# Performance work log

Measured on AMD Instinct MI355X. Metric: run time of the kernel, lower is better.

The kernel has to match this reference:

```python
import jax, jax.numpy as jnp
import numpy as np

B, H, S, D = 2048, 1024, 32768, 64  # batch, hidden_dim, memory_slots, slot_size


def setup_inputs() -> dict:
    key = jax.random.key(0)
    ks = jax.random.split(key, 8)
    inp = {
        "query": jax.random.normal(ks[0], (B, H), jnp.float32),
        "consciousness_level": jax.random.uniform(ks[1], (B,), jnp.float32),
        "content": jax.random.normal(ks[2], (B, H), jnp.float32),
        "memory": jax.random.normal(ks[3], (S, D), jnp.float32) * 0.1,
        "memory_age": jnp.zeros((S,), jnp.float32),
        "memory_strength": jnp.ones((S,), jnp.float32) * 0.1,
        "W_read": jax.random.normal(ks[4], (H + 1, S), jnp.float32) / np.sqrt(H + 1),
        "b_read": jnp.zeros((S,), jnp.float32),
        "W_write": jax.random.normal(ks[5], (H + 1, S), jnp.float32) / np.sqrt(H + 1),
        "b_write": jnp.zeros((S,), jnp.float32),
        "W_cp": jax.random.normal(ks[6], (H, D), jnp.float32) / np.sqrt(H),
        "b_cp": jnp.zeros((D,), jnp.float32),
        "W_ce": jax.random.normal(ks[7], (D, H), jnp.float32) / np.sqrt(D),
        "b_ce": jnp.zeros((H,), jnp.float32),
    }
    return inp


def reference(query, consciousness_level, content, memory, memory_age,
              memory_strength, W_read, b_read, W_write, b_write,
              W_cp, b_cp, W_ce, b_ce):
    # ---- read path ----
    enhanced_query = jnp.concatenate([query, consciousness_level[:, None]], axis=-1)  # [B, H+1]
    read_weights = jax.nn.softmax(enhanced_query @ W_read + b_read, axis=-1)          # [B, S]
    boosted = read_weights * memory_strength[None, :]
    boosted = boosted / (boosted.sum(axis=-1, keepdims=True) + 1e-6)
    read_content = boosted @ memory                                                   # [B, D]
    consciousness_boost = read_content @ W_ce + b_ce                                  # [B, H]

    # ---- write path (vectorized masked consolidation over all slots) ----
    c_mean = consciousness_level.mean()
    write_weights = jax.nn.softmax(enhanced_query @ W_write + b_write, axis=-1)       # [B, S]
    ww_mean = write_weights.mean(axis=0)                                              # [S]
    pc_mean = (content @ W_cp + b_cp).mean(axis=0)                                    # [D]
    weight = ww_mean * (c_mean * 2.0)                                                 # [S]
    gate = c_mean >= 0.3                                                              # auto-activation threshold
    mask = (weight > 0.005) & gate                                                    # [S] bool
    consolidation = jax.nn.sigmoid(memory_age * 0.1 + c_mean)                         # [S]
    alpha = weight * consolidation                                                    # [S]
    new_memory = jnp.where(mask[:, None],
                           (1.0 - alpha)[:, None] * memory + alpha[:, None] * pc_mean[None, :],
                           memory)                                                    # [S, D]
    new_age = memory_age + mask.astype(memory_age.dtype)
    new_strength = jnp.where(mask,
                             jnp.clip(memory_strength + weight * 0.1, 0.1, 2.0),
                             memory_strength)
    return read_content, consciousness_boost, new_memory, new_age, new_strength
```

## Files before the change

### kernel.cpp

```cpp
#include <hip/hip_runtime.h>
#include <hip/hip_bf16.h>
#include <cstdint>
#include <cstddef>

#define B_ 2048
#define H_ 1024
#define S_ 32768
#define D_ 64
#define BT 32
#define KQ 1024
#define NT 16
#define KP 1088

typedef unsigned char u8;
typedef unsigned short u16;
typedef __attribute__((ext_vector_type(8))) short bf16x8;
typedef __attribute__((ext_vector_type(8))) unsigned short ushort8v;
typedef __attribute__((ext_vector_type(4))) float f32x4;

#define WS_CMEAN      0
#define WS_PCMEAN     64
#define WS_CMM        128
#define WS_ZR         (WS_CMM + H_)
#define WS_TR         (WS_ZR + B_)
#define WS_VR         (WS_TR + B_)
#define WS_ZW         (WS_VR + B_*D_)
#define WS_WWM        (WS_ZW + B_)
#define WS_END        (WS_WWM + S_)

__device__ __forceinline__ u16 f2bf(float f) {
  unsigned u = __float_as_uint(f);
  unsigned r = (u + 0x7FFFu + ((u >> 16) & 1u)) >> 16;
  return (u16)r;
}

__device__ __forceinline__ float bf2f(u16 v) {
  return __uint_as_float(((unsigned)v) << 16);
}

__device__ __forceinline__ u8 f8enc(float f) {
  f = fminf(f, 448.f);
  unsigned u = __float_as_uint(f);
  int ex = (int)((u >> 23) & 255) - 127;
  unsigned r;
  if (ex >= -6) {
    unsigned m = u & 0x7FFFFF;
    unsigned rm = (m + 0x7FFFF + ((m >> 20) & 1)) >> 20;
    r = ((unsigned)(ex + 7) << 3) + rm;
  } else {
    r = (unsigned)fminf(7.f, f * 512.f + 0.5f);
  }
  return (u8)(r > 126 ? 126 : r);
}

__device__ __forceinline__ float f8dec(u8 b) {
  int ef = (b >> 3) & 15, m = b & 7;
  return ef ? __uint_as_float(((unsigned)(ef + 120) << 23) | ((unsigned)m << 20))
            : (float)m * 0.001953125f;
}

__device__ __forceinline__ void gload_lds16(const void* g, void* l) {
  __builtin_amdgcn_global_load_lds(
      (const __attribute__((address_space(1))) unsigned int*)g,
      (__attribute__((address_space(3))) unsigned int*)l, 16, 0, 0);
}


__global__ void k_pre(const float* __restrict__ query, const float* __restrict__ cl,
                      const float* __restrict__ content, const float* __restrict__ mem,
                      const float* __restrict__ Wr, const float* __restrict__ Ww,
                      u16* __restrict__ qb, u16* __restrict__ mT,
                      u16* __restrict__ wbtR, u16* __restrict__ wbtW,
                      float* __restrict__ ws) {
  const int blk = blockIdx.x, t = threadIdx.x;
  if (blk < 128) {
    const int h = (blk & 3) * 256 + t;
    const int b0 = (blk >> 2) * 64;
    float acc = 0.f;
    #pragma unroll 8
    for (int b = 0; b < 64; ++b) acc += content[(size_t)(b0 + b) * H_ + h];
    atomicAdd(&ws[WS_CMM + h], acc * (1.0f / B_));
  } else if (blk < 160) {
    if (t < 64) {
      float acc = cl[(blk - 128) * 64 + t];
      #pragma unroll
      for (int off = 32; off > 0; off >>= 1) acc += __shfl_down(acc, off);
      if (t == 0) atomicAdd(&ws[WS_CMEAN], acc * (1.0f / B_));
    }
  } else if (blk < 160 + B_) {
    const int b = blk - 160;
    const float4 q4 = *reinterpret_cast<const float4*>(&query[(size_t)b * H_ + t * 4]);
    ushort4 o;
    o.x = f2bf(q4.x); o.y = f2bf(q4.y); o.z = f2bf(q4.z); o.w = f2bf(q4.w);
    *reinterpret_cast<ushort4*>(&qb[(size_t)b * KQ + t * 4]) = o;
  } else if (blk < 160 + B_ + 512) {
    __shared__ float tile[64][65];
    const int s0 = (blk - 160 - B_) * 64;
    const int c = t & 63, rbase = t >> 6;
    #pragma unroll
    for (int i = 0; i < 16; ++i) {
      const int r = rbase + i * 4;
      tile[r][c] = mem[(size_t)(s0 + r) * D_ + c];
    }
    __syncthreads();
    #pragma unroll
    for (int i = 0; i < 16; ++i) {
      const int d = rbase + i * 4;
      mT[(size_t)d * S_ + s0 + c] = f2bf(tile[c][d]);
    }
  } else {
    const int base = 160 + B_ + 512;
    const int isW = blk >= base + 8192;
    const int i = blk - base - (isW ? 8192 : 0);
    const float* __restrict__ W = isW ? Ww : Wr;
    u16* __restrict__ wbt = isW ? wbtW : wbtR;
    __shared__ float tile[64][65];
    const int s0 = (i & 511) * 64;
    const int k0 = (i >> 9) * 64;
    const int c = t & 63, rbase = t >> 6;
    #pragma unroll
    for (int j = 0; j < 16; ++j) {
      const int r = rbase + j * 4;
      tile[r][c] = W[(size_t)(k0 + r) * S_ + s0 + c];
    }
    __syncthreads();
    #pragma unroll
    for (int j = 0; j < 16; ++j) {
      const int sr = rbase + j * 4;
      wbt[(size_t)(s0 + sr) * KQ + k0 + c] = f2bf(tile[c][sr]);
    }
  }
}

template <int NF>
__device__ __forceinline__ void rd_frags(const u16* __restrict__ lds, int rowbase,
                                         int lr, int lg, bf16x8 (&dst)[NF * 2]) {
  #pragma unroll
  for (int f = 0; f < NF; ++f) {
    const int rr = rowbase + f * 16 + lr;
    #pragma unroll
    for (int ks = 0; ks < 2; ++ks) {
      const int ch = (ks * 4 + lg) ^ (rr & 7);
      dst[f * 2 + ks] = *(const bf16x8*)&lds[rr * 64 + ch * 8];
    }
  }
}

template <int QR, int QC>
__device__ __forceinline__ void mfmaq(f32x4 (&acc)[8][4], const bf16x8 (&av)[8],
                                      const bf16x8 (&bv)[4]) {
  #pragma unroll
  for (int m16 = 0; m16 < 4; ++m16)
    #pragma unroll
    for (int n16 = 0; n16 < 2; ++n16)
      #pragma unroll
      for (int ks = 0; ks < 2; ++ks)
        acc[QR * 4 + m16][QC * 2 + n16] = __builtin_amdgcn_mfma_f32_16x16x32_bf16(
            av[m16 * 2 + ks], bv[n16 * 2 + ks], acc[QR * 4 + m16][QC * 2 + n16], 0, 0, 0);
}

template <int VARIANT>
__global__ __launch_bounds__(512, 2) void k_gemm(
    const u16* __restrict__ qb, const u16* __restrict__ wbt,
    const float* __restrict__ Wfull, const float* __restrict__ biasv,
    const float* __restrict__ cl, const float* __restrict__ strength,
    const u16* __restrict__ mT, void* __restrict__ pout, float* __restrict__ ws) {
  __shared__ __align__(16) u16 SMEM[4][256 * 64];
  const int t = threadIdx.x;
  const int w = t >> 6, l = t & 63;
  const int wm = w >> 2, wn = w & 3;
  const int lr = l & 15, lg = l >> 4;

  const int lin = blockIdx.x + 8 * blockIdx.y;
  const int xcd = lin & 7, idx = lin >> 3;
  const size_t r0 = (size_t)(idx & 7) * 256;
  const int cblk = xcd * 16 + (idx >> 3);
  const size_t c0 = (size_t)cblk * 256;

  f32x4 acc[8][4];
  #pragma unroll
  for (int m = 0; m < 8; ++m)
    #pragma unroll
    for (int n = 0; n < 4; ++n) acc[m][n] = (f32x4)0.f;

  auto STAGE = [&](int kt2, int pp) {
    #pragma unroll
    for (int i = 0; i < 4; ++i) {
      const int q = i * 512 + t;
      const int r = q >> 3;
      const int sc = (q & 7) ^ (r & 7);
      gload_lds16(qb + (r0 + r) * KQ + (size_t)kt2 * 64 + sc * 8, &SMEM[pp][q * 8]);
    }
    #pragma unroll
    for (int i = 0; i < 4; ++i) {
      const int q = i * 512 + t;
      const int r = q >> 3;
      const int sc = (q & 7) ^ (r & 7);
      gload_lds16(wbt + (c0 + r) * KQ + (size_t)kt2 * 64 + sc * 8, &SMEM[2 + pp][q * 8]);
    }
  };

  STAGE(0, 0);
  STAGE(1, 1);
  asm volatile("s_waitcnt vmcnt(8)" ::: "memory");
  __builtin_amdgcn_sched_barrier(0);
  __builtin_amdgcn_s_barrier();

  for (int kt = 0; kt < NT; ++kt) {
    const int p = kt & 1;
    const u16* __restrict__ Ap = &SMEM[p][0];
    const u16* __restrict__ Bp = &SMEM[2 + p][0];
    bf16x8 a[8], b0[4], b1[4];
    rd_frags<4>(Ap, wm * 128 + 0, lr, lg, a);
    rd_frags<2>(Bp, wn * 64 + 0, lr, lg, b0);
    __builtin_amdgcn_sched_barrier(0);
    __builtin_amdgcn_s_barrier();
    __builtin_amdgcn_s_setprio(1);
    mfmaq<0, 0>(acc, a, b0);
    __builtin_amdgcn_s_setprio(0);
    __builtin_amdgcn_s_barrier();
    rd_frags<2>(Bp, wn * 64 + 32, lr, lg, b1);
    __builtin_amdgcn_sched_barrier(0);
    __builtin_amdgcn_s_barrier();
    __builtin_amdgcn_s_setprio(1);
    mfmaq<0, 1>(acc, a, b1);
    __builtin_amdgcn_s_setprio(0);
    __builtin_amdgcn_s_barrier();
    rd_frags<4>(Ap, wm * 128 + 64, lr, lg, a);
    __builtin_amdgcn_sched_barrier(0);
    __builtin_amdgcn_s_barrier();
    __builtin_amdgcn_s_setprio(1);
    mfmaq<1, 1>(acc, a, b1);
    __builtin_amdgcn_s_setprio(0);
    __builtin_amdgcn_s_barrier();
    if (kt + 2 < NT) STAGE(kt + 2, p);
    __builtin_amdgcn_s_barrier();
    __builtin_amdgcn_s_setprio(1);
    mfmaq<1, 0>(acc, a, b0);
    __builtin_amdgcn_s_setprio(0);
    if (kt + 2 < NT) {
      asm volatile("s_waitcnt vmcnt(8)" ::: "memory");
    } else if (kt + 1 < NT) {
      asm volatile("s_waitcnt vmcnt(0)" ::: "memory");
    }
    __builtin_amdgcn_sched_barrier(0);
    __builtin_amdgcn_s_barrier();
  }

  float wl4[4], bb4[4];
  #pragma unroll
  for (int n = 0; n < 4; ++n) {
    const size_t col = c0 + wn * 64 + n * 16 + lr;
    wl4[n] = Wfull[(size_t)H_ * S_ + col];
    bb4[n] = biasv[col];
  }
  #pragma unroll
  for (int m = 0; m < 8; ++m) {
    #pragma unroll
    for (int j = 0; j < 4; ++j) {
      const float clv = cl[r0 + wm * 128 + m * 16 + lg * 4 + j];
      #pragma unroll
      for (int n = 0; n < 4; ++n)
        acc[m][n][j] += fmaf(clv, wl4[n], bb4[n]);
    }
  }

  u16* __restrict__ Plds = &SMEM[0][0];

  if (VARIANT == 0) {
    float st4[4];
    #pragma unroll
    for (int n = 0; n < 4; ++n) st4[n] = strength[c0 + wn * 64 + n * 16 + lr];
    #pragma unroll
    for (int m = 0; m < 8; ++m) {
      #pragma unroll
      for (int j = 0; j < 4; ++j) {
        const int rloc = wm * 128 + m * 16 + lg * 4 + j;
        float ze = 0.f, zp = 0.f;
        #pragma unroll
        for (int n = 0; n < 4; ++n) {
          const float e = __expf(acc[m][n][j]);
          const float pq = e * st4[n];
          ze += e;
          zp += pq;
          const int col = wn * 64 + n * 16 + lr;
          const int ch = (col >> 3) ^ (rloc & 7);
          Plds[rloc * 256 + ch * 8 + (col & 7)] = f2bf(pq);
        }
        #pragma unroll
        for (int off = 1; off < 16; off <<= 1) {
          ze += __shfl_xor(ze, off);
          zp += __shfl_xor(zp, off);
        }
        if (lr == 0) {
          atomicAdd(&ws[WS_ZR + r0 + rloc], ze);
          atomicAdd(&ws[WS_TR + r0 + rloc], zp);
        }
      }
    }
    __syncthreads();
    float* __restrict__ vp = (float*)pout;
    f32x4 pv[2][4];
    #pragma unroll
    for (int f = 0; f < 2; ++f)
      #pragma unroll
      for (int n = 0; n < 4; ++n) pv[f][n] = (f32x4)0.f;
    #pragma unroll 2
    for (int ks = 0; ks < 8; ++ks) {
      bf16x8 pa[2], pb[4];
      #pragma unroll
      for (int f = 0; f < 2; ++f) {
        const int row = w * 32 + f * 16 + lr;
        const int ch = (ks * 4 + lg) ^ (row & 7);
        pa[f] = *(const bf16x8*)&Plds[row * 256 + ch * 8];
      }
      #pragma unroll
      for (int n = 0; n < 4; ++n)
        pb[n] = *(const bf16x8*)&mT[(size_t)(n * 16 + lr) * S_ + c0 + ks * 32 + lg * 8];
      #pragma unroll
      for (int f = 0; f < 2; ++f)
        #pragma unroll
        for (int n = 0; n < 4; ++n)
          pv[f][n] = __builtin_amdgcn_mfma_f32_16x16x32_bf16(pa[f], pb[n], pv[f][n], 0, 0, 0);
    }
    #pragma unroll
    for (int f = 0; f < 2; ++f) {
      #pragma unroll
      for (int j = 0; j < 4; ++j) {
        const size_t R = (size_t)cblk * B_ + r0 + w * 32 + f * 16 + lg * 4 + j;
        #pragma unroll
        for (int n = 0; n < 4; ++n)
          vp[R * 64 + n * 16 + lr] = pv[f][n][j];
      }
    }
  } else {
    #pragma unroll
    for (int m = 0; m < 8; ++m) {
      #pragma unroll
      for (int j = 0; j < 4; ++j) {
        const int rloc = wm * 128 + m * 16 + lg * 4 + j;
        #pragma unroll
        for (int n = 0; n < 4; ++n) {
          const int col = wn * 64 + n * 16 + lr;
          const int ch = (col >> 3) ^ (rloc & 7);
          Plds[rloc * 256 + ch * 8 + (col & 7)] = f2bf(__expf(acc[m][n][j]));
        }
      }
    }
    __syncthreads();
    u8* __restrict__ pout8 = (u8*)pout;
    #pragma unroll 2
    for (int it = 0; it < 8; ++it) {
      const int row = w * 32 + it * 4 + (l >> 4);
      const int c2 = (l & 15) * 2;
      const bf16x8 e0 = *(const bf16x8*)&Plds[row * 256 + ((c2 ^ (row & 7)) * 8)];
      const bf16x8 e1 = *(const bf16x8*)&Plds[row * 256 + (((c2 + 1) ^ (row & 7)) * 8)];
      float ze = 0.f;
      uint4 fb;
      unsigned wds[4] = {0, 0, 0, 0};
      #pragma unroll
      for (int q = 0; q < 8; ++q) {
        const float ea = bf2f((u16)e0[q]);
        const float eb = bf2f((u16)e1[q]);
        ze += ea + eb;
        wds[q >> 2] |= ((unsigned)f8enc(ea)) << ((q & 3) * 8);
        wds[2 + (q >> 2)] |= ((unsigned)f8enc(eb)) << ((q & 3) * 8);
      }
      fb.x = wds[0]; fb.y = wds[1]; fb.z = wds[2]; fb.w = wds[3];
      *(uint4*)&pout8[(r0 + row) * S_ + c0 + (size_t)(l & 15) * 16] = fb;
      #pragma unroll
      for (int off = 1; off < 16; off <<= 1) ze += __shfl_xor(ze, off);
      if ((l & 15) == 0) atomicAdd(&ws[WS_ZW + r0 + row], ze);
    }
  }
}

__global__ void k_rc2cb(const float* __restrict__ vp, const float* __restrict__ Wcp,
                        const float* __restrict__ bcp, const float* __restrict__ Wce,
                        const float* __restrict__ bce, float* __restrict__ ws,
                        float* __restrict__ out_rc, float* __restrict__ out_cb) {
  const int t = threadIdx.x;
  if (blockIdx.x == 512) {
    __shared__ float red[4][64];
    const int d = t & 63, kk = t >> 6;
    float acc = 0.f;
    #pragma unroll 8
    for (int k = kk * 256; k < kk * 256 + 256; ++k)
      acc = fmaf(ws[WS_CMM + k], Wcp[(size_t)k * D_ + d], acc);
    red[kk][d] = acc;
    __syncthreads();
    if (t < 64) {
      float a = bcp[t];
      #pragma unroll
      for (int i = 0; i < 4; ++i) a += red[i][t];
      ws[WS_PCMEAN + t] = a;
    }
    return;
  }
  __shared__ float rcs[4][64];
  const int idx = blockIdx.x * 256 + t;
  const int b = idx >> 6, d = idx & 63;
  float v = 0.f;
  #pragma unroll 4
  for (int c = 0; c < 128; ++c) v += vp[(size_t)c * B_ * 64 + idx];
  const float rcv = v / (ws[WS_TR + b] + 1e-6f * ws[WS_ZR + b]);
  out_rc[idx] = rcv;
  rcs[t >> 6][d] = rcv;
  __syncthreads();
  const int b0 = blockIdx.x * 4;
  #pragma unroll
  for (int oo = 0; oo < 4; ++oo) {
    const int h = oo * 256 + t;
    float a0 = bce[h], a1 = a0, a2 = a0, a3 = a0;
    #pragma unroll 8
    for (int dd = 0; dd < 64; ++dd) {
      const float wv = Wce[(size_t)dd * H_ + h];
      a0 = fmaf(rcs[0][dd], wv, a0);
      a1 = fmaf(rcs[1][dd], wv, a1);
      a2 = fmaf(rcs[2][dd], wv, a2);
      a3 = fmaf(rcs[3][dd], wv, a3);
    }
    out_cb[(size_t)(b0 + 0) * H_ + h] = a0;
    out_cb[(size_t)(b0 + 1) * H_ + h] = a1;
    out_cb[(size_t)(b0 + 2) * H_ + h] = a2;
    out_cb[(size_t)(b0 + 3) * H_ + h] = a3;
  }
}


__global__ void k_wwm_f8(const u8* __restrict__ ebuf, float* __restrict__ ws) {
  const int t = threadIdx.x;
  const int s0 = blockIdx.x * 4096 + t * 16;
  const int b0 = blockIdx.y * 128;
  float ww[16];
  #pragma unroll
  for (int j = 0; j < 16; ++j) ww[j] = 0.f;
  #pragma unroll 1
  for (int b = 0; b < 128; ++b) {
    const float inv = 1.0f / ws[WS_ZW + b0 + b];
    const uint4 v = *reinterpret_cast<const uint4*>(&ebuf[(size_t)(b0 + b) * S_ + s0]);
    const unsigned vv[4] = {v.x, v.y, v.z, v.w};
    #pragma unroll
    for (int j = 0; j < 16; ++j) {
      const u8 byte = (u8)((vv[j >> 2] >> ((j & 3) * 8)) & 0xFF);
      ww[j] = fmaf(f8dec(byte), inv, ww[j]);
    }
  }
  #pragma unroll
  for (int j = 0; j < 16; ++j) atomicAdd(&ws[WS_WWM + s0 + j], ww[j]);
}

__global__ void k_final(const float* __restrict__ mem, const float* __restrict__ age,
                        const float* __restrict__ strength, const float* __restrict__ ws,
                        float* __restrict__ out_mem, float* __restrict__ out_age,
                        float* __restrict__ out_str) {
  const int idx = blockIdx.x * 256 + threadIdx.x;
  const int s = idx >> 6, dd = idx & 63;
  const float cm = ws[WS_CMEAN];
  const float w = ws[WS_WWM + s] * (2.0f * cm / B_);
  const bool mask = (w > 0.005f) && (cm >= 0.3f);
  float m = mem[idx];
  if (mask) {
    const float cons = 1.0f / (1.0f + __expf(-(age[s] * 0.1f + cm)));
    const float alpha = w * cons;
    m = (1.0f - alpha) * m + alpha * ws[WS_PCMEAN + dd];
  }
  out_mem[idx] = m;
  if (dd == 0) {
    out_age[s] = age[s] + (mask ? 1.0f : 0.0f);
    out_str[s] = mask ? fminf(fmaxf(strength[s] + w * 0.1f, 0.1f), 2.0f) : strength[s];
  }
}


__global__ void k_stats(const float* __restrict__ content,
                        const float* __restrict__ cl, float* __restrict__ ws) {
  const int gx = blockIdx.x, gy = blockIdx.y, t = threadIdx.x;
  if (gx < 4) {
    const int h = gx * 256 + t;
    const int b0 = gy * 64;
    float acc = 0.f;
    #pragma unroll 8
    for (int b = 0; b < 64; ++b) acc += content[(size_t)(b0 + b) * H_ + h];
    atomicAdd(&ws[WS_CMM + h], acc * (1.0f / B_));
  } else if (t < 64) {
    float acc = cl[gy * 64 + t];
    #pragma unroll
    for (int off = 32; off > 0; off >>= 1) acc += __shfl_down(acc, off);
    if (t == 0) atomicAdd(&ws[WS_CMEAN], acc * (1.0f / B_));
  }
}

__global__ void k_pcmean(const float* __restrict__ Wcp, const float* __restrict__ bcp,
                         float* __restrict__ ws) {
  __shared__ float red[16][64];
  const int t = threadIdx.x, d = t & 63, kk = t >> 6;
  float acc = 0.f;
  const int k0 = kk * 64;
  #pragma unroll 8
  for (int k = k0; k < k0 + 64; ++k)
    acc = fmaf(ws[WS_CMM + k], Wcp[(size_t)k * D_ + d], acc);
  red[kk][d] = acc;
  __syncthreads();
  if (t < 64) {
    float a = bcp[t];
    #pragma unroll
    for (int i = 0; i < 16; ++i) a += red[i][t];
    ws[WS_PCMEAN + t] = a;
  }
}

template <int NR>
__device__ __forceinline__ void logits_kloop(const float* __restrict__ q, int row0,
                                             const float* __restrict__ W, int s,
                                             float* acc) {
  #pragma unroll 1
  for (int k = 0; k < H_; k += 4) {
    const float w0 = W[(size_t)(k + 0) * S_ + s];
    const float w1 = W[(size_t)(k + 1) * S_ + s];
    const float w2 = W[(size_t)(k + 2) * S_ + s];
    const float w3 = W[(size_t)(k + 3) * S_ + s];
    #pragma unroll
    for (int r = 0; r < NR; ++r) {
      const float4 qv = *reinterpret_cast<const float4*>(&q[(size_t)(row0 + r) * H_ + k]);
      float a = acc[r];
      a = fmaf(qv.x, w0, a);
      a = fmaf(qv.y, w1, a);
      a = fmaf(qv.z, w2, a);
      a = fmaf(qv.w, w3, a);
      acc[r] = a;
    }
  }
}

__global__ __launch_bounds__(512, 2) void k_read(
    const float* __restrict__ q, const float* __restrict__ cl,
    const float* __restrict__ Wr, const float* __restrict__ br,
    const float* __restrict__ strength, const float* __restrict__ mem,
    float* __restrict__ ws) {
  __shared__ float plds[BT * 512];
  const int t = threadIdx.x;
  const int r0 = blockIdx.x * BT;
  const int squar = blockIdx.y;
  const int d = t & 63, wv = t >> 6;

  float zacc[BT], tacc[BT];
  #pragma unroll
  for (int r = 0; r < BT; ++r) { zacc[r] = 0.f; tacc[r] = 0.f; }
  float vacc[4] = {0.f, 0.f, 0.f, 0.f};

  for (int tile = 0; tile < 16; ++tile) {
    const int sg0 = squar * 8192 + tile * 512;
    const int s = sg0 + t;
    float acc[BT];
    const float wlast = Wr[(size_t)H_ * S_ + s];
    const float bias = br[s];
    #pragma unroll
    for (int r = 0; r < BT; ++r) acc[r] = fmaf(cl[r0 + r], wlast, bias);
    logits_kloop<BT>(q, r0, Wr, s, acc);

    const float stg = strength[s];
    #pragma unroll
    for (int r = 0; r < BT; ++r) {
      const float e = __expf(acc[r]);
      zacc[r] += e;
      const float p = e * stg;
      tacc[r] += p;
      plds[r * 512 + t] = p;
    }
    __syncthreads();
    #pragma unroll 1
    for (int sl = 0; sl < 512; sl += 4) {
      const float m0 = mem[(size_t)(sg0 + sl + 0) * D_ + d];
      const float m1 = mem[(size_t)(sg0 + sl + 1) * D_ + d];
      const float m2 = mem[(size_t)(sg0 + sl + 2) * D_ + d];
      const float m3 = mem[(size_t)(sg0 + sl + 3) * D_ + d];
      #pragma unroll
      for (int j = 0; j < 4; ++j) {
        const float4 pv = *reinterpret_cast<const float4*>(&plds[(wv + 8 * j) * 512 + sl]);
        float v = vacc[j];
        v = fmaf(pv.x, m0, v);
        v = fmaf(pv.y, m1, v);
        v = fmaf(pv.z, m2, v);
        v = fmaf(pv.w, m3, v);
        vacc[j] = v;
      }
    }
    __syncthreads();
  }

  float* red0 = plds;
  float* red1 = plds + 8 * BT;
  #pragma unroll
  for (int r = 0; r < BT; ++r) {
    float z = zacc[r], tt = tacc[r];
    #pragma unroll
    for (int off = 32; off > 0; off >>= 1) {
      z += __shfl_down(z, off);
      tt += __shfl_down(tt, off);
    }
    if ((t & 63) == 0) { red0[wv * BT + r] = z; red1[wv * BT + r] = tt; }
  }
  __syncthreads();
  if (t < BT) {
    float z = 0.f, tt = 0.f;
    #pragma unroll
    for (int wq = 0; wq < 8; ++wq) { z += red0[wq * BT + t]; tt += red1[wq * BT + t]; }
    atomicAdd(&ws[WS_ZR + r0 + t], z);
    atomicAdd(&ws[WS_TR + r0 + t], tt);
  }
  #pragma unroll
  for (int j = 0; j < 4; ++j)
    atomicAdd(&ws[WS_VR + (size_t)(r0 + wv + 8 * j) * D_ + d], vacc[j]);
}

__global__ __launch_bounds__(512, 2) void k_write_pass1(
    const float* __restrict__ q, const float* __restrict__ cl,
    const float* __restrict__ Ww, const float* __restrict__ bw,
    float* __restrict__ ws, __hip_bfloat16* __restrict__ ebuf, const int store_e) {
  __shared__ float red[8 * BT];
  const int t = threadIdx.x;
  const int r0 = blockIdx.x * BT;
  const int squar = blockIdx.y;
  const int wv = t >> 6;

  float zacc[BT];
  #pragma unroll
  for (int r = 0; r < BT; ++r) zacc[r] = 0.f;

  for (int tile = 0; tile < 16; ++tile) {
    const int s = squar * 8192 + tile * 512 + t;
    float acc[BT];
    const float wlast = Ww[(size_t)H_ * S_ + s];
    const float bias = bw[s];
    #pragma unroll
    for (int r = 0; r < BT; ++r) acc[r] = fmaf(cl[r0 + r], wlast, bias);
    logits_kloop<BT>(q, r0, Ww, s, acc);
    #pragma unroll
    for (int r = 0; r < BT; ++r) {
      const float e = __expf(acc[r]);
      zacc[r] += e;
      if (store_e) ebuf[(size_t)(r0 + r) * S_ + s] = __float2bfloat16(e);
    }
  }
  #pragma unroll
  for (int r = 0; r < BT; ++r) {
    float z = zacc[r];
    #pragma unroll
    for (int off = 32; off > 0; off >>= 1) z += __shfl_down(z, off);
    if ((t & 63) == 0) red[wv * BT + r] = z;
  }
  __syncthreads();
  if (t < BT) {
    float z = 0.f;
    #pragma unroll
    for (int wq = 0; wq < 8; ++wq) z += red[wq * BT + t];
    atomicAdd(&ws[WS_ZW + r0 + t], z);
  }
}

__global__ void k_rc(const float* __restrict__ ws, float* __restrict__ out) {
  const int idx = blockIdx.x * 256 + threadIdx.x;
  const int b = idx >> 6;
  const float z = ws[WS_ZR + b], tt = ws[WS_TR + b];
  out[idx] = ws[WS_VR + idx] / (tt + 1e-6f * z);
}

__global__ void k_cboost(const float* __restrict__ rc, const float* __restrict__ Wce,
                         const float* __restrict__ bce, float* __restrict__ out) {
  const int idx = blockIdx.x * 256 + threadIdx.x;
  const int b = idx >> 10, h = idx & 1023;
  const float* __restrict__ rcb = &rc[b * 64];
  float acc = bce[h];
  #pragma unroll
  for (int dd = 0; dd < 64; dd += 4) {
    const float4 r4 = *reinterpret_cast<const float4*>(&rcb[dd]);
    acc = fmaf(r4.x, Wce[(size_t)(dd + 0) * H_ + h], acc);
    acc = fmaf(r4.y, Wce[(size_t)(dd + 1) * H_ + h], acc);
    acc = fmaf(r4.z, Wce[(size_t)(dd + 2) * H_ + h], acc);
    acc = fmaf(r4.w, Wce[(size_t)(dd + 3) * H_ + h], acc);
  }
  out[idx] = acc;
}

__global__ void k_wwm_store(const __hip_bfloat16* __restrict__ ebuf,
                            float* __restrict__ ws) {
  const int t = threadIdx.x;
  const int s0 = blockIdx.x * 2048 + t * 8;
  const int b0 = blockIdx.y * 128;
  const u16* __restrict__ eb = (const u16*)ebuf;
  float ww[8];
  #pragma unroll
  for (int j = 0; j < 8; ++j) ww[j] = 0.f;
  #pragma unroll 1
  for (int b = 0; b < 128; ++b) {
    const float inv = 1.0f / ws[WS_ZW + b0 + b];
    const ushort8v ev = *reinterpret_cast<const ushort8v*>(&eb[(size_t)(b0 + b) * S_ + s0]);
    #pragma unroll
    for (int j = 0; j < 8; ++j) {
      const float e = __uint_as_float(((unsigned)ev[j]) << 16);
      ww[j] = fmaf(e, inv, ww[j]);
    }
  }
  #pragma unroll
  for (int j = 0; j < 8; ++j) atomicAdd(&ws[WS_WWM + s0 + j], ww[j]);
}

__global__ __launch_bounds__(512, 2) void k_wwm_recompute(
    const float* __restrict__ q, const float* __restrict__ cl,
    const float* __restrict__ Ww, const float* __restrict__ bw,
    float* __restrict__ ws) {
  const int t = threadIdx.x;
  const int s = blockIdx.x * 512 + t;
  const int b0 = blockIdx.y * 256;
  const float wlast = Ww[(size_t)H_ * S_ + s];
  const float bias = bw[s];
  float wwacc = 0.f;
  for (int g = 0; g < 8; ++g) {
    const int rb = b0 + g * 32;
    float acc[BT];
    #pragma unroll
    for (int r = 0; r < BT; ++r) acc[r] = fmaf(cl[rb + r], wlast, bias);
    logits_kloop<BT>(q, rb, Ww, s, acc);
    #pragma unroll
    for (int r = 0; r < BT; ++r) wwacc += __expf(acc[r]) / ws[WS_ZW + rb + r];
  }
  atomicAdd(&ws[WS_WWM + s], wwacc);
}


extern "C" void kernel_launch(void* const* d_in, const int* in_sizes, int n_in,
                              void* d_out, int out_size, void* d_ws, size_t ws_size,
                              hipStream_t stream) {
  const float* query    = (const float*)d_in[0];
  const float* cl       = (const float*)d_in[1];
  const float* content  = (const float*)d_in[2];
  const float* memory   = (const float*)d_in[3];
  const float* age      = (const float*)d_in[4];
  const float* strength = (const float*)d_in[5];
  const float* W_read   = (const float*)d_in[6];
  const float* b_read   = (const float*)d_in[7];
  const float* W_write  = (const float*)d_in[8];
  const float* b_write  = (const float*)d_in[9];
  const float* W_cp     = (const float*)d_in[10];
  const float* b_cp     = (const float*)d_in[11];
  const float* W_ce     = (const float*)d_in[12];
  const float* b_ce     = (const float*)d_in[13];

  float* out = (float*)d_out;
  float* ws = (float*)d_ws;
  float* out_rc  = out;
  float* out_cb  = out + B_ * D_;
  float* out_mem = out_cb + (size_t)B_ * H_;
  float* out_age = out_mem + (size_t)S_ * D_;
  float* out_str = out_age + S_;

  const size_t QB_F    = WS_END;
  const size_t MEMT_F  = QB_F + (size_t)B_ * KQ / 2;
  const size_t WBTR_F  = MEMT_F + (size_t)D_ * S_ / 2;
  const size_t WBTW_F  = WBTR_F + (size_t)S_ * KQ / 2;
  const size_t PBUF_F  = WBTW_F + (size_t)S_ * KQ / 2;
  const size_t FAST_END_F = PBUF_F + (size_t)128 * B_ * 64;

  hipMemsetAsync(ws, 0, (size_t)WS_END * sizeof(float), stream);

  if (ws_size >= FAST_END_F * sizeof(float)) {
    u16* qb   = (u16*)(ws + QB_F);
    u16* mT   = (u16*)(ws + MEMT_F);
    u16* wbtR = (u16*)(ws + WBTR_F);
    u16* wbtW = (u16*)(ws + WBTW_F);
    float* vp = (float*)(ws + PBUF_F);
    u8*  pf8  = (u8*)(ws + PBUF_F);

    k_pre<<<160 + B_ + 512 + 2 * 8192, 256, 0, stream>>>(
        query, cl, content, memory, W_read, W_write, qb, mT, wbtR, wbtW, ws);
    k_gemm<0><<<dim3(8, 128), 512, 0, stream>>>(qb, wbtR, W_read, b_read, cl,
                                                strength, mT, (void*)vp, ws);
    k_rc2cb<<<513, 256, 0, stream>>>(vp, W_cp, b_cp, W_ce, b_ce, ws, out_rc, out_cb);
    k_gemm<1><<<dim3(8, 128), 512, 0, stream>>>(qb, wbtW, W_write, b_write, cl,
                                                nullptr, mT, (void*)pf8, ws);
    k_wwm_f8<<<dim3(8, 16), 256, 0, stream>>>(pf8, ws);
    k_final<<<(S_ * D_) / 256, 256, 0, stream>>>(memory, age, strength, ws,
                                                 out_mem, out_age, out_str);
  } else {
    const size_t ebuf_bytes = (size_t)B_ * S_ * 2;
    const int store_e = (ws_size >= (size_t)WS_END * 4 + ebuf_bytes) ? 1 : 0;
    __hip_bfloat16* ebuf = (__hip_bfloat16*)(ws + WS_END);

    k_stats<<<dim3(5, 32), 256, 0, stream>>>(content, cl, ws);
    k_pcmean<<<1, 1024, 0, stream>>>(W_cp, b_cp, ws);
    k_read<<<dim3(B_ / BT, 4), 512, 0, stream>>>(query, cl, W_read, b_read, strength, memory, ws);
    k_write_pass1<<<dim3(B_ / BT, 4), 512, 0, stream>>>(query, cl, W_write, b_write, ws, ebuf, store_e);
    k_rc<<<(B_ * D_) / 256, 256, 0, stream>>>(ws, out_rc);
    k_cboost<<<(B_ * H_) / 256, 256, 0, stream>>>(out_rc, W_ce, b_ce, out_cb);
    if (store_e) {
      k_wwm_store<<<dim3(S_ / 2048, B_ / 128), 256, 0, stream>>>(ebuf, ws);
    } else {
      k_wwm_recompute<<<dim3(S_ / 512, 8), 512, 0, stream>>>(query, cl, W_write, b_write, ws);
    }
    k_final<<<(S_ * D_) / 256, 256, 0, stream>>>(memory, age, strength, ws,
                                                 out_mem, out_age, out_str);
  }
}
```

Baseline: 667.7 us.

## Materialize bf16 read probabilities and split P@memory into separate kernel

The read GEMM no longer computes P@memory in its epilogue. It writes the bf16 probability matrix to global memory, reduces softmax row sums in LDS before the global atomics, and a new k_pv kernel computes P@memory with MFMA and atomically accumulates into the workspace. The W_write transpose moves into its own kernel that reuses the W_read bf16 buffer, and the row stride is padded to 1056 to avoid channel or bank conflicts. This shrinks the workspace and drops the 128-way partial-sum buffer, but adds a 128MB round trip of P through memory plus extra launches and atomics.

```diff
diff --git a/kernel.cpp b/kernel.cpp
--- a/kernel.cpp
+++ b/kernel.cpp
@@ -9,8 +9,8 @@
 #define D_ 64
 #define BT 32
 #define KQ 1024
+#define KQS 1056
 #define NT 16
-#define KP 1088
 
 typedef unsigned char u8;
 typedef unsigned short u16;
@@ -68,10 +68,9 @@
 
 __global__ void k_pre(const float* __restrict__ query, const float* __restrict__ cl,
                       const float* __restrict__ content, const float* __restrict__ mem,
-                      const float* __restrict__ Wr, const float* __restrict__ Ww,
+                      const float* __restrict__ Wr,
                       u16* __restrict__ qb, u16* __restrict__ mT,
-                      u16* __restrict__ wbtR, u16* __restrict__ wbtW,
-                      float* __restrict__ ws) {
+                      u16* __restrict__ wbtR, float* __restrict__ ws) {
   const int blk = blockIdx.x, t = threadIdx.x;
   if (blk < 128) {
     const int h = (blk & 3) * 256 + t;
@@ -92,7 +91,7 @@
     const float4 q4 = *reinterpret_cast<const float4*>(&query[(size_t)b * H_ + t * 4]);
     ushort4 o;
     o.x = f2bf(q4.x); o.y = f2bf(q4.y); o.z = f2bf(q4.z); o.w = f2bf(q4.w);
-    *reinterpret_cast<ushort4*>(&qb[(size_t)b * KQ + t * 4]) = o;
+    *reinterpret_cast<ushort4*>(&qb[(size_t)b * KQS + t * 4]) = o;
   } else if (blk < 160 + B_ + 512) {
     __shared__ float tile[64][65];
     const int s0 = (blk - 160 - B_) * 64;
@@ -109,11 +108,7 @@
       mT[(size_t)d * S_ + s0 + c] = f2bf(tile[c][d]);
     }
   } else {
-    const int base = 160 + B_ + 512;
-    const int isW = blk >= base + 8192;
-    const int i = blk - base - (isW ? 8192 : 0);
-    const float* __restrict__ W = isW ? Ww : Wr;
-    u16* __restrict__ wbt = isW ? wbtW : wbtR;
+    const int i = blk - (160 + B_ + 512);
     __shared__ float tile[64][65];
     const int s0 = (i & 511) * 64;
     const int k0 = (i >> 9) * 64;
@@ -121,14 +116,33 @@
     #pragma unroll
     for (int j = 0; j < 16; ++j) {
       const int r = rbase + j * 4;
-      tile[r][c] = W[(size_t)(k0 + r) * S_ + s0 + c];
+      tile[r][c] = Wr[(size_t)(k0 + r) * S_ + s0 + c];
     }
     __syncthreads();
     #pragma unroll
     for (int j = 0; j < 16; ++j) {
       const int sr = rbase + j * 4;
-      wbt[(size_t)(s0 + sr) * KQ + k0 + c] = f2bf(tile[c][sr]);
-    }
+      wbtR[(size_t)(s0 + sr) * KQS + k0 + c] = f2bf(tile[c][sr]);
+    }
+  }
+}
+
+__global__ void k_cvt_wtW(const float* __restrict__ W, u16* __restrict__ wbt) {
+  __shared__ float tile[64][65];
+  const int t = threadIdx.x;
+  const int s0 = blockIdx.x * 64;
+  const int k0 = blockIdx.y * 64;
+  const int c = t & 63, rbase = t >> 6;
+  #pragma unroll
+  for (int j = 0; j < 16; ++j) {
+    const int r = rbase + j * 4;
+    tile[r][c] = W[(size_t)(k0 + r) * S_ + s0 + c];
+  }
+  __syncthreads();
+  #pragma unroll
+  for (int j = 0; j < 16; ++j) {
+    const int sr = rbase + j * 4;
+    wbt[(size_t)(s0 + sr) * KQS + k0 + c] = f2bf(tile[c][sr]);
   }
 }
 
@@ -164,7 +178,7 @@
     const u16* __restrict__ qb, const u16* __restrict__ wbt,
     const float* __restrict__ Wfull, const float* __restrict__ biasv,
     const float* __restrict__ cl, const float* __restrict__ strength,
-    const u16* __restrict__ mT, void* __restrict__ pout, float* __restrict__ ws) {
+    void* __restrict__ pout, float* __restrict__ ws) {
   __shared__ __align__(16) u16 SMEM[4][256 * 64];
   const int t = threadIdx.x;
   const int w = t >> 6, l = t & 63;
@@ -189,14 +203,14 @@
       const int q = i * 512 + t;
       const int r = q >> 3;
       const int sc = (q & 7) ^ (r & 7);
-      gload_lds16(qb + (r0 + r) * KQ + (size_t)kt2 * 64 + sc * 8, &SMEM[pp][q * 8]);
+      gload_lds16(qb + (r0 + r) * KQS + (size_t)kt2 * 64 + sc * 8, &SMEM[pp][q * 8]);
     }
     #pragma unroll
     for (int i = 0; i < 4; ++i) {
       const int q = i * 512 + t;
       const int r = q >> 3;
       const int sc = (q & 7) ^ (r & 7);
-      gload_lds16(wbt + (c0 + r) * KQ + (size_t)kt2 * 64 + sc * 8, &SMEM[2 + pp][q * 8]);
+      gload_lds16(wbt + (c0 + r) * KQS + (size_t)kt2 * 64 + sc * 8, &SMEM[2 + pp][q * 8]);
     }
   };
 
@@ -265,9 +279,12 @@
     }
   }
 
-  u16* __restrict__ Plds = &SMEM[0][0];
-
   if (VARIANT == 0) {
+    float* zred = (float*)&SMEM[0][0];
+    float* tred = zred + 256;
+    if (t < 512) zred[t] = 0.f;
+    __syncthreads();
+    u16* __restrict__ pout16 = (u16*)pout;
     float st4[4];
     #pragma unroll
     for (int n = 0; n < 4; ++n) st4[n] = strength[c0 + wn * 64 + n * 16 + lr];
@@ -276,64 +293,38 @@
       #pragma unroll
       for (int j = 0; j < 4; ++j) {
         const int rloc = wm * 128 + m * 16 + lg * 4 + j;
+        const size_t R = r0 + rloc;
         float ze = 0.f, zp = 0.f;
+        u16 pb[4];
         #pragma unroll
         for (int n = 0; n < 4; ++n) {
           const float e = __expf(acc[m][n][j]);
           const float pq = e * st4[n];
           ze += e;
           zp += pq;
-          const int col = wn * 64 + n * 16 + lr;
-          const int ch = (col >> 3) ^ (rloc & 7);
-          Plds[rloc * 256 + ch * 8 + (col & 7)] = f2bf(pq);
+          pb[n] = f2bf(pq);
         }
+        #pragma unroll
+        for (int n = 0; n < 4; ++n)
+          pout16[R * S_ + c0 + wn * 64 + n * 16 + lr] = pb[n];
         #pragma unroll
         for (int off = 1; off < 16; off <<= 1) {
           ze += __shfl_xor(ze, off);
           zp += __shfl_xor(zp, off);
         }
         if (lr == 0) {
-          atomicAdd(&ws[WS_ZR + r0 + rloc], ze);
-          atomicAdd(&ws[WS_TR + r0 + rloc], zp);
+          atomicAdd(&zred[rloc], ze);
+          atomicAdd(&tred[rloc], zp);
         }
       }
     }
     __syncthreads();
-    float* __restrict__ vp = (float*)pout;
-    f32x4 pv[2][4];
-    #pragma unroll
-    for (int f = 0; f < 2; ++f)
-      #pragma unroll
-      for (int n = 0; n < 4; ++n) pv[f][n] = (f32x4)0.f;
-    #pragma unroll 2
-    for (int ks = 0; ks < 8; ++ks) {
-      bf16x8 pa[2], pb[4];
-      #pragma unroll
-      for (int f = 0; f < 2; ++f) {
-        const int row = w * 32 + f * 16 + lr;
-        const int ch = (ks * 4 + lg) ^ (row & 7);
-        pa[f] = *(const bf16x8*)&Plds[row * 256 + ch * 8];
-      }
-      #pragma unroll
-      for (int n = 0; n < 4; ++n)
-        pb[n] = *(const bf16x8*)&mT[(size_t)(n * 16 + lr) * S_ + c0 + ks * 32 + lg * 8];
-      #pragma unroll
-      for (int f = 0; f < 2; ++f)
-        #pragma unroll
-        for (int n = 0; n < 4; ++n)
-          pv[f][n] = __builtin_amdgcn_mfma_f32_16x16x32_bf16(pa[f], pb[n], pv[f][n], 0, 0, 0);
-    }
-    #pragma unroll
-    for (int f = 0; f < 2; ++f) {
-      #pragma unroll
-      for (int j = 0; j < 4; ++j) {
-        const size_t R = (size_t)cblk * B_ + r0 + w * 32 + f * 16 + lg * 4 + j;
-        #pragma unroll
-        for (int n = 0; n < 4; ++n)
-          vp[R * 64 + n * 16 + lr] = pv[f][n][j];
-      }
+    if (t < 256) {
+      atomicAdd(&ws[WS_ZR + r0 + t], zred[t]);
+      atomicAdd(&ws[WS_TR + r0 + t], tred[t]);
     }
   } else {
+    u16* __restrict__ Plds = &SMEM[0][0];
     #pragma unroll
     for (int m = 0; m < 8; ++m) {
       #pragma unroll
@@ -375,9 +366,52 @@
   }
 }
 
-__global__ void k_rc2cb(const float* __restrict__ vp, const float* __restrict__ Wcp,
-                        const float* __restrict__ bcp, const float* __restrict__ Wce,
-                        const float* __restrict__ bce, float* __restrict__ ws,
+__global__ void k_pv(const u16* __restrict__ P, const u16* __restrict__ mT,
+                     float* __restrict__ ws) {
+  __shared__ float Vs[64 * 64];
+  const int t = threadIdx.x;
+  const int w = t >> 6, l = t & 63;
+  const int lr = l & 15, lg = l >> 4;
+  const size_t r0 = (size_t)blockIdx.x * 64;
+  const size_t s0 = (size_t)blockIdx.y * 1024 + (size_t)w * 256;
+  f32x4 acc[4][4];
+  #pragma unroll
+  for (int m = 0; m < 4; ++m)
+    #pragma unroll
+    for (int n = 0; n < 4; ++n) acc[m][n] = (f32x4)0.f;
+
+  for (int ks = 0; ks < 8; ++ks) {
+    const size_t sb = s0 + ks * 32 + lg * 8;
+    bf16x8 a[4], b[4];
+    #pragma unroll
+    for (int m = 0; m < 4; ++m)
+      a[m] = *(const bf16x8*)&P[(r0 + m * 16 + lr) * S_ + sb];
+    #pragma unroll
+    for (int n = 0; n < 4; ++n)
+      b[n] = *(const bf16x8*)&mT[(size_t)(n * 16 + lr) * S_ + sb];
+    #pragma unroll
+    for (int m = 0; m < 4; ++m)
+      #pragma unroll
+      for (int n = 0; n < 4; ++n)
+        acc[m][n] = __builtin_amdgcn_mfma_f32_16x16x32_bf16(a[m], b[n], acc[m][n], 0, 0, 0);
+  }
+  for (int i = t; i < 4096; i += 256) Vs[i] = 0.f;
+  __syncthreads();
+  #pragma unroll
+  for (int m = 0; m < 4; ++m)
+    #pragma unroll
+    for (int j = 0; j < 4; ++j)
+      #pragma unroll
+      for (int n = 0; n < 4; ++n)
+        atomicAdd(&Vs[(m * 16 + lg * 4 + j) * 64 + n * 16 + lr], acc[m][n][j]);
+  __syncthreads();
+  for (int i = t; i < 4096; i += 256)
+    atomicAdd(&ws[WS_VR + (r0 + (size_t)(i >> 6)) * 64 + (i & 63)], Vs[i]);
+}
+
+__global__ void k_rc2cb(const float* __restrict__ Wcp, const float* __restrict__ bcp,
+                        const float* __restrict__ Wce, const float* __restrict__ bce,
+                        float* __restrict__ ws,
                         float* __restrict__ out_rc, float* __restrict__ out_cb) {
   const int t = threadIdx.x;
   if (blockIdx.x == 512) {
@@ -400,10 +434,7 @@
   __shared__ float rcs[4][64];
   const int idx = blockIdx.x * 256 + t;
   const int b = idx >> 6, d = idx & 63;
-  float v = 0.f;
-  #pragma unroll 4
-  for (int c = 0; c < 128; ++c) v += vp[(size_t)c * B_ * 64 + idx];
-  const float rcv = v / (ws[WS_TR + b] + 1e-6f * ws[WS_ZR + b]);
+  const float rcv = ws[WS_VR + idx] / (ws[WS_TR + b] + 1e-6f * ws[WS_ZR + b]);
   out_rc[idx] = rcv;
   rcs[t >> 6][d] = rcv;
   __syncthreads();
@@ -756,11 +787,10 @@
   float* out_str = out_age + S_;
 
   const size_t QB_F    = WS_END;
-  const size_t MEMT_F  = QB_F + (size_t)B_ * KQ / 2;
+  const size_t MEMT_F  = QB_F + (size_t)B_ * KQS / 2;
   const size_t WBTR_F  = MEMT_F + (size_t)D_ * S_ / 2;
-  const size_t WBTW_F  = WBTR_F + (size_t)S_ * KQ / 2;
-  const size_t PBUF_F  = WBTW_F + (size_t)S_ * KQ / 2;
-  const size_t FAST_END_F = PBUF_F + (size_t)128 * B_ * 64;
+  const size_t PBUF_F  = WBTR_F + (size_t)S_ * KQS / 2;
+  const size_t FAST_END_F = PBUF_F + (size_t)B_ * S_ / 2;
 
   hipMemsetAsync(ws, 0, (size_t)WS_END * sizeof(float), stream);
 
@@ -768,17 +798,18 @@
     u16* qb   = (u16*)(ws + QB_F);
     u16* mT   = (u16*)(ws + MEMT_F);
     u16* wbtR = (u16*)(ws + WBTR_F);
-    u16* wbtW = (u16*)(ws + WBTW_F);
-    float* vp = (float*)(ws + PBUF_F);
+    u16* pbuf = (u16*)(ws + PBUF_F);
     u8*  pf8  = (u8*)(ws + PBUF_F);
 
-    k_pre<<<160 + B_ + 512 + 2 * 8192, 256, 0, stream>>>(
-        query, cl, content, memory, W_read, W_write, qb, mT, wbtR, wbtW, ws);
+    k_pre<<<160 + B_ + 512 + 8192, 256, 0, stream>>>(
+        query, cl, content, memory, W_read, qb, mT, wbtR, ws);
     k_gemm<0><<<dim3(8, 128), 512, 0, stream>>>(qb, wbtR, W_read, b_read, cl,
-                                                strength, mT, (void*)vp, ws);
-    k_rc2cb<<<513, 256, 0, stream>>>(vp, W_cp, b_cp, W_ce, b_ce, ws, out_rc, out_cb);
-    k_gemm<1><<<dim3(8, 128), 512, 0, stream>>>(qb, wbtW, W_write, b_write, cl,
-                                                nullptr, mT, (void*)pf8, ws);
+                                                strength, (void*)pbuf, ws);
+    k_cvt_wtW<<<dim3(512, 16), 256, 0, stream>>>(W_write, wbtR);
+    k_pv<<<dim3(B_ / 64, 32), 256, 0, stream>>>(pbuf, mT, ws);
+    k_rc2cb<<<513, 256, 0, stream>>>(W_cp, b_cp, W_ce, b_ce, ws, out_rc, out_cb);
+    k_gemm<1><<<dim3(8, 128), 512, 0, stream>>>(qb, wbtR, W_write, b_write, cl,
+                                                nullptr, (void*)pf8, ws);
     k_wwm_f8<<<dim3(8, 16), 256, 0, stream>>>(pf8, ws);
     k_final<<<(S_ * D_) / 256, 256, 0, stream>>>(memory, age, strength, ws,
                                                  out_mem, out_age, out_str);
```

After: 761.1 us. +14.0%, slower.
